# Performance work log

Hardware: AMD Instinct MI355X
Metric: run time of the kernel (lower is better)

## Reference

```python
import jax, jax.numpy as jnp
import numpy as np


def setup_inputs() -> dict:
    key = jax.random.key(0)
    k1, k2, k3 = jax.random.split(key, 3)
    B, C_in, H, W = 16, 256, 64, 64
    C_out, KH, KW = 256, 3, 3
    x = jax.random.normal(k1, (B, C_in, H, W), dtype=jnp.float32)
    # kaiming-uniform-like scale for realism
    fan_in = C_in * KH * KW
    bound = 1.0 / np.sqrt(fan_in)
    weights = jax.random.normal(k2, (C_out, C_in, KH, KW), dtype=jnp.float32) * bound
    bias = jax.random.uniform(k3, (C_out,), dtype=jnp.float32, minval=-bound, maxval=bound)
    return {"x": x, "weights": weights, "bias": bias}


def reference(x, weights, bias):
    # Conv2dApproximation with approximation_enable=False is an exact conv2d:
    # input is unfolded to [B, C*kh*kw, oh, ow], weights to [C_out, C*kh*kw],
    # and the MultiApp kernel performs the exact MAC (see exact matmul backward).
    # stride=(1,1), padding=(0,0), dilation=(1,1) per init_kwargs.
    out = jax.lax.conv_general_dilated(
        x, weights,
        window_strides=(1, 1),
        padding=((0, 0), (0, 0)),
        rhs_dilation=(1, 1),
        dimension_numbers=("NCHW", "OIHW", "NCHW"),
    )
    return out + bias[None, :, None, None]
```

## Files before the change

### kernel.cpp

```cpp
#include <hip/hip_runtime.h>
#include <stdint.h>

typedef short short8 __attribute__((ext_vector_type(8)));
typedef float f32x4 __attribute__((ext_vector_type(4)));

#define AS1 __attribute__((address_space(1)))
#define AS3 __attribute__((address_space(3)))

__device__ __forceinline__ void gl_lds16(const void* g, void* l) {
  __builtin_amdgcn_global_load_lds((const AS1 unsigned int*)g,
                                   (AS3 unsigned int*)l, 16, 0, 0);
}

__device__ __forceinline__ unsigned short f2bf(float f) {
  union { float f; unsigned int u; } v; v.f = f;
  return (unsigned short)((v.u + (((v.u >> 16) & 1u) + 0x7fffu)) >> 16);
}

__global__ __launch_bounds__(256) void xpose_kernel(const float* __restrict__ x,
                                                    unsigned short* __restrict__ xt) {
  __shared__ float tile[64][68];
  const int bid = blockIdx.x;
  const int cchunk = bid & 3;
  const int y = (bid >> 2) & 63;
  const int b = bid >> 8;
  const int t = threadIdx.x;
  const int ci0 = cchunk * 64;

  const int cc = t >> 2;
  const int xo = (t & 3) * 16;
  const float* src = x + (((size_t)(b * 256 + ci0 + cc) * 64 + y) * 64 + xo);
  float4 v0 = ((const float4*)src)[0];
  float4 v1 = ((const float4*)src)[1];
  float4 v2 = ((const float4*)src)[2];
  float4 v3 = ((const float4*)src)[3];
  *(float4*)&tile[cc][xo + 0]  = v0;
  *(float4*)&tile[cc][xo + 4]  = v1;
  *(float4*)&tile[cc][xo + 8]  = v2;
  *(float4*)&tile[cc][xo + 12] = v3;
  __syncthreads();

  const int xpos = t >> 2;
  const int ccg = (t & 3) * 16;
  unsigned int pk[8];
#pragma unroll
  for (int e = 0; e < 8; ++e) {
    unsigned int lo = f2bf(tile[ccg + 2 * e][xpos]);
    unsigned int hi = f2bf(tile[ccg + 2 * e + 1][xpos]);
    pk[e] = lo | (hi << 16);
  }
  unsigned short* dst = xt + ((size_t)(b * 4096 + y * 64 + xpos) * 256 + ci0 + ccg);
  uint4 w0; w0.x = pk[0]; w0.y = pk[1]; w0.z = pk[2]; w0.w = pk[3];
  uint4 w1; w1.x = pk[4]; w1.y = pk[5]; w1.z = pk[6]; w1.w = pk[7];
  ((uint4*)dst)[0] = w0;
  ((uint4*)dst)[1] = w1;
}

__global__ __launch_bounds__(256) void wpack_kernel(const float* __restrict__ w,
                                                    unsigned short* __restrict__ wrp) {
  const int idx = blockIdx.x * 256 + threadIdx.x;
  const int ci = idx & 255;
  const int co = (idx >> 8) & 255;
  const int p = idx >> 16;
  wrp[idx] = f2bf(w[(size_t)(co * 256 + ci) * 9 + p]);
}

__global__ __launch_bounds__(512, 2) void conv_8ph(
    const unsigned short* __restrict__ xt,
    const unsigned short* __restrict__ wrp,
    const float* __restrict__ bias,
    float* __restrict__ out) {
  __shared__ unsigned short lds[2][32768];

  const int tid = threadIdx.x;
  const int lane = tid & 63;
  const int wv = tid >> 6;
  const int wm = wv >> 2;
  const int wn = wv & 3;
  const int bid = blockIdx.x;
  const int tile = (bid & 7) * 32 + (bid >> 3);
  const int b = tile >> 4;
  const int oh0 = (tile & 15) * 4;

  const int crow = tid >> 3;
  const int cslot = tid & 7;
  const int sw = cslot ^ (crow & 7);
  const unsigned short* gAbase = wrp + (size_t)crow * 256 + sw * 8;
  const unsigned short* gBbase[4];
#pragma unroll
  for (int cb = 0; cb < 4; ++cb) {
    const int y = min(oh0 + cb, 61);
    const int x = min(crow, 61);
    gBbase[cb] = xt + ((size_t)(b * 64 + y) * 64 + x) * 256 + sw * 8;
  }
  const unsigned dst_rc = crow * 64 + cslot * 8;

  const int l15 = lane & 15;
  int s8[2];
  s8[0] = (((lane >> 4)) ^ (lane & 7)) * 8;
  s8[1] = (((lane >> 4) + 4) ^ (lane & 7)) * 8;
  int arow[8], brow[4];
#pragma unroll
  for (int a = 0; a < 8; ++a)
    arow[a] = (wm * 128 + (a >> 2) * 64 + (a & 3) * 16 + l15) * 64;
#pragma unroll
  for (int n = 0; n < 4; ++n)
    brow[n] = 16384 + (wn * 64 + n * 16 + l15) * 64;

  auto stageA = [&](int kt2, int c, unsigned short* bufp) {
    const int tap = kt2 >> 2, ci0 = (kt2 & 3) * 64;
    gl_lds16(gAbase + tap * 65536 + c * 16384 + ci0, bufp + c * 4096 + dst_rc);
  };
  auto stageB = [&](int kt2, int cb, unsigned short* bufp) {
    const int tap = kt2 >> 2, ci0 = (kt2 & 3) * 64;
    const int kh = (tap * 11) >> 5, kw = tap - kh * 3;
    gl_lds16(gBbase[cb] + (kh * 64 + kw) * 256 + ci0, bufp + (4 + cb) * 4096 + dst_rc);
  };

  f32x4 acc[8][4] = {};
  unsigned short* buf0 = &lds[0][0];
  unsigned short* buf1 = &lds[1][0];

  stageA(0, 0, buf0); stageA(0, 2, buf0); stageA(0, 1, buf0); stageA(0, 3, buf0);
  stageB(0, 2, buf0); stageB(0, 3, buf0); stageB(0, 0, buf0); stageB(0, 1, buf0);
  stageB(1, 0, buf1); stageB(1, 1, buf1);
  asm volatile("s_waitcnt vmcnt(2)" ::: "memory");
  __builtin_amdgcn_s_barrier();

  for (int kt = 0; kt < 36; ++kt) {
    unsigned short* buf = (kt & 1) ? buf1 : buf0;
    unsigned short* nbuf = (kt & 1) ? buf0 : buf1;
    short8 a0[4], a1[4], bb[4];

#pragma unroll
    for (int q = 0; q < 4; ++q) a0[q] = *(const short8*)(buf + arow[q] + s8[0]);
#pragma unroll
    for (int n = 0; n < 4; ++n) bb[n] = *(const short8*)(buf + brow[n] + s8[0]);
    if (kt < 35) { stageA(kt + 1, 0, nbuf); stageA(kt + 1, 2, nbuf); }
    __builtin_amdgcn_s_barrier();
    __builtin_amdgcn_s_setprio(1);
#pragma unroll
    for (int q = 0; q < 4; ++q)
#pragma unroll
      for (int n = 0; n < 4; ++n)
        acc[q][n] = __builtin_amdgcn_mfma_f32_16x16x32_bf16(a0[q], bb[n], acc[q][n], 0, 0, 0);
    __builtin_amdgcn_s_setprio(0);
    asm volatile("s_waitcnt lgkmcnt(0)" ::: "memory");
    __builtin_amdgcn_s_barrier();

#pragma unroll
    for (int q = 0; q < 4; ++q) a1[q] = *(const short8*)(buf + arow[4 + q] + s8[0]);
    if (kt < 35) { stageA(kt + 1, 1, nbuf); stageA(kt + 1, 3, nbuf); }
    __builtin_amdgcn_s_barrier();
    __builtin_amdgcn_s_setprio(1);
#pragma unroll
    for (int q = 0; q < 4; ++q)
#pragma unroll
      for (int n = 0; n < 4; ++n)
        acc[4 + q][n] = __builtin_amdgcn_mfma_f32_16x16x32_bf16(a1[q], bb[n], acc[4 + q][n], 0, 0, 0);
    __builtin_amdgcn_s_setprio(0);
    asm volatile("s_waitcnt lgkmcnt(0)" ::: "memory");
    __builtin_amdgcn_s_barrier();

#pragma unroll
    for (int q = 0; q < 4; ++q) a0[q] = *(const short8*)(buf + arow[q] + s8[1]);
#pragma unroll
    for (int n = 0; n < 4; ++n) bb[n] = *(const short8*)(buf + brow[n] + s8[1]);
    if (kt < 35) { stageB(kt + 1, 2, nbuf); stageB(kt + 1, 3, nbuf); }
    __builtin_amdgcn_s_barrier();
    __builtin_amdgcn_s_setprio(1);
#pragma unroll
    for (int q = 0; q < 4; ++q)
#pragma unroll
      for (int n = 0; n < 4; ++n)
        acc[q][n] = __builtin_amdgcn_mfma_f32_16x16x32_bf16(a0[q], bb[n], acc[q][n], 0, 0, 0);
    __builtin_amdgcn_s_setprio(0);
    asm volatile("s_waitcnt lgkmcnt(0)" ::: "memory");
    __builtin_amdgcn_s_barrier();

#pragma unroll
    for (int q = 0; q < 4; ++q) a1[q] = *(const short8*)(buf + arow[4 + q] + s8[1]);
    if (kt < 34) { stageB(kt + 2, 0, buf); stageB(kt + 2, 1, buf); }
    __builtin_amdgcn_s_barrier();
    __builtin_amdgcn_s_setprio(1);
#pragma unroll
    for (int q = 0; q < 4; ++q)
#pragma unroll
      for (int n = 0; n < 4; ++n)
        acc[4 + q][n] = __builtin_amdgcn_mfma_f32_16x16x32_bf16(a1[q], bb[n], acc[4 + q][n], 0, 0, 0);
    __builtin_amdgcn_s_setprio(0);
    asm volatile("s_waitcnt lgkmcnt(0)" ::: "memory");
    if (kt < 34)       asm volatile("s_waitcnt vmcnt(2)" ::: "memory");
    else if (kt == 34) asm volatile("s_waitcnt vmcnt(0)" ::: "memory");
    __builtin_amdgcn_s_barrier();
  }

  const int rb = (lane >> 4) * 4;
  const int colp = lane & 15;
#pragma unroll
  for (int a = 0; a < 8; ++a) {
    const int co = wm * 128 + (a >> 2) * 64 + (a & 3) * 16 + rb;
    float bv[4];
#pragma unroll
    for (int j = 0; j < 4; ++j) bv[j] = bias[co + j];
#pragma unroll
    for (int n = 0; n < 4; ++n) {
      const int px = wn * 64 + n * 16 + colp;
      const int prow = px >> 6, ow = px & 63;
      const int oh = oh0 + prow;
      if (ow < 62 && oh < 62) {
#pragma unroll
        for (int j = 0; j < 4; ++j)
          out[((size_t)(b * 256 + co + j) * 62 + oh) * 62 + ow] = acc[a][n][j] + bv[j];
      }
    }
  }
}

__global__ __launch_bounds__(256) void conv_naive(const float* __restrict__ x,
                                                  const float* __restrict__ wgt,
                                                  const float* __restrict__ bias,
                                                  float* __restrict__ out) {
  const size_t idx = (size_t)blockIdx.x * 256 + threadIdx.x;
  if (idx >= (size_t)16 * 256 * 62 * 62) return;
  const int ow = (int)(idx % 62);
  size_t r = idx / 62;
  const int oh = (int)(r % 62); r /= 62;
  const int co = (int)(r % 256);
  const int b = (int)(r / 256);
  float s = bias[co];
  for (int ci = 0; ci < 256; ++ci) {
    const float* xp = x + ((size_t)(b * 256 + ci) * 64 + oh) * 64 + ow;
    const float* wp = wgt + (size_t)(co * 256 + ci) * 9;
#pragma unroll
    for (int kh = 0; kh < 3; ++kh)
#pragma unroll
      for (int kw = 0; kw < 3; ++kw)
        s += xp[kh * 64 + kw] * wp[kh * 3 + kw];
  }
  out[idx] = s;
}

extern "C" void kernel_launch(void* const* d_in, const int* in_sizes, int n_in,
                              void* d_out, int out_size, void* d_ws, size_t ws_size,
                              hipStream_t stream) {
  const float* x = (const float*)d_in[0];
  const float* wgt = (const float*)d_in[1];
  const float* bias = (const float*)d_in[2];
  float* out = (float*)d_out;

  const size_t xt_elems = (size_t)16 * 64 * 64 * 256;
  const size_t wr_elems = (size_t)9 * 256 * 256;
  const size_t need = (xt_elems + wr_elems) * sizeof(unsigned short);

  if (ws_size < need) {
    conv_naive<<<61504, 256, 0, stream>>>(x, wgt, bias, out);
    return;
  }

  unsigned short* xt = (unsigned short*)d_ws;
  unsigned short* wrp = xt + xt_elems;

  xpose_kernel<<<4096, 256, 0, stream>>>(x, xt);
  wpack_kernel<<<2304, 256, 0, stream>>>(wgt, wrp);
  conv_8ph<<<256, 512, 0, stream>>>(xt, wrp, bias, out);
}
```

Measured before the change: 97.53 us.

## Load conv B operand directly into registers and triple-buffer A in LDS

The input-activation (B) fragments now go straight from global memory into registers, each wave fetching its own pixels, and are double-buffered two k-tiles ahead. Only the weight (A) tile is still staged in LDS, now across three rotating buffers. This cuts LDS traffic and drops the sync points from four barriers per k-tile to one, letting MFMA issue run with fewer stalls. In exchange, waves that share the same B columns fetch them redundantly from cache, two register buffers of B fragments add pressure under the 2-block launch bound, and the vmcnt accounting has to match the new load counts exactly.

```diff
diff --git a/kernel.cpp b/kernel.cpp
--- a/kernel.cpp
+++ b/kernel.cpp
@@ -65,12 +65,12 @@
   wrp[idx] = f2bf(w[(size_t)(co * 256 + ci) * 9 + p]);
 }
 
-__global__ __launch_bounds__(512, 2) void conv_8ph(
+__global__ __launch_bounds__(512, 2) void conv_breg(
     const unsigned short* __restrict__ xt,
     const unsigned short* __restrict__ wrp,
     const float* __restrict__ bias,
     float* __restrict__ out) {
-  __shared__ unsigned short lds[2][32768];
+  __shared__ unsigned short lds[3 * 16384];
 
   const int tid = threadIdx.x;
   const int lane = tid & 63;
@@ -86,113 +86,99 @@
   const int cslot = tid & 7;
   const int sw = cslot ^ (crow & 7);
   const unsigned short* gAbase = wrp + (size_t)crow * 256 + sw * 8;
-  const unsigned short* gBbase[4];
-#pragma unroll
-  for (int cb = 0; cb < 4; ++cb) {
-    const int y = min(oh0 + cb, 61);
-    const int x = min(crow, 61);
-    gBbase[cb] = xt + ((size_t)(b * 64 + y) * 64 + x) * 256 + sw * 8;
-  }
-  const unsigned dst_rc = crow * 64 + cslot * 8;
+  const unsigned dstA = crow * 64 + cslot * 8;
 
   const int l15 = lane & 15;
-  int s8[2];
-  s8[0] = (((lane >> 4)) ^ (lane & 7)) * 8;
-  s8[1] = (((lane >> 4) + 4) ^ (lane & 7)) * 8;
-  int arow[8], brow[4];
-#pragma unroll
-  for (int a = 0; a < 8; ++a)
-    arow[a] = (wm * 128 + (a >> 2) * 64 + (a & 3) * 16 + l15) * 64;
-#pragma unroll
-  for (int n = 0; n < 4; ++n)
-    brow[n] = 16384 + (wn * 64 + n * 16 + l15) * 64;
-
-  auto stageA = [&](int kt2, int c, unsigned short* bufp) {
+  const int kq = lane >> 4;
+  const int s8k0 = ((kq) ^ (lane & 7)) * 8;
+  const int s8k1 = ((kq + 4) ^ (lane & 7)) * 8;
+
+  const unsigned short* pB[4];
+#pragma unroll
+  for (int n = 0; n < 4; ++n) {
+    const int px = wn * 64 + n * 16 + l15;
+    const int y = min(oh0 + (px >> 6), 61);
+    const int xc = min(px & 63, 61);
+    pB[n] = xt + ((size_t)(b * 64 + y) * 64 + xc) * 256 + kq * 8;
+  }
+
+  auto stageA = [&](int kt2, unsigned short* pst) {
     const int tap = kt2 >> 2, ci0 = (kt2 & 3) * 64;
-    gl_lds16(gAbase + tap * 65536 + c * 16384 + ci0, bufp + c * 4096 + dst_rc);
+    const unsigned short* g = gAbase + tap * 65536 + ci0;
+#pragma unroll
+    for (int c = 0; c < 4; ++c)
+      gl_lds16(g + c * 16384, pst + c * 4096 + dstA);
   };
-  auto stageB = [&](int kt2, int cb, unsigned short* bufp) {
+  auto loadB = [&](int kt2, short8 (&dst)[4][2]) {
     const int tap = kt2 >> 2, ci0 = (kt2 & 3) * 64;
     const int kh = (tap * 11) >> 5, kw = tap - kh * 3;
-    gl_lds16(gBbase[cb] + (kh * 64 + kw) * 256 + ci0, bufp + (4 + cb) * 4096 + dst_rc);
+    const int boff = (kh * 64 + kw) * 256 + ci0;
+#pragma unroll
+    for (int n = 0; n < 4; ++n) {
+      dst[n][0] = *(const short8*)(pB[n] + boff);
+      dst[n][1] = *(const short8*)(pB[n] + boff + 32);
+    }
   };
 
   f32x4 acc[8][4] = {};
-  unsigned short* buf0 = &lds[0][0];
-  unsigned short* buf1 = &lds[1][0];
-
-  stageA(0, 0, buf0); stageA(0, 2, buf0); stageA(0, 1, buf0); stageA(0, 3, buf0);
-  stageB(0, 2, buf0); stageB(0, 3, buf0); stageB(0, 0, buf0); stageB(0, 1, buf0);
-  stageB(1, 0, buf1); stageB(1, 1, buf1);
-  asm volatile("s_waitcnt vmcnt(2)" ::: "memory");
-  __builtin_amdgcn_s_barrier();
-
-  for (int kt = 0; kt < 36; ++kt) {
-    unsigned short* buf = (kt & 1) ? buf1 : buf0;
-    unsigned short* nbuf = (kt & 1) ? buf0 : buf1;
-    short8 a0[4], a1[4], bb[4];
-
-#pragma unroll
-    for (int q = 0; q < 4; ++q) a0[q] = *(const short8*)(buf + arow[q] + s8[0]);
-#pragma unroll
-    for (int n = 0; n < 4; ++n) bb[n] = *(const short8*)(buf + brow[n] + s8[0]);
-    if (kt < 35) { stageA(kt + 1, 0, nbuf); stageA(kt + 1, 2, nbuf); }
-    __builtin_amdgcn_s_barrier();
-    __builtin_amdgcn_s_setprio(1);
-#pragma unroll
-    for (int q = 0; q < 4; ++q)
-#pragma unroll
-      for (int n = 0; n < 4; ++n)
-        acc[q][n] = __builtin_amdgcn_mfma_f32_16x16x32_bf16(a0[q], bb[n], acc[q][n], 0, 0, 0);
-    __builtin_amdgcn_s_setprio(0);
-    asm volatile("s_waitcnt lgkmcnt(0)" ::: "memory");
-    __builtin_amdgcn_s_barrier();
-
-#pragma unroll
-    for (int q = 0; q < 4; ++q) a1[q] = *(const short8*)(buf + arow[4 + q] + s8[0]);
-    if (kt < 35) { stageA(kt + 1, 1, nbuf); stageA(kt + 1, 3, nbuf); }
-    __builtin_amdgcn_s_barrier();
-    __builtin_amdgcn_s_setprio(1);
-#pragma unroll
-    for (int q = 0; q < 4; ++q)
-#pragma unroll
-      for (int n = 0; n < 4; ++n)
-        acc[4 + q][n] = __builtin_amdgcn_mfma_f32_16x16x32_bf16(a1[q], bb[n], acc[4 + q][n], 0, 0, 0);
-    __builtin_amdgcn_s_setprio(0);
-    asm volatile("s_waitcnt lgkmcnt(0)" ::: "memory");
-    __builtin_amdgcn_s_barrier();
-
-#pragma unroll
-    for (int q = 0; q < 4; ++q) a0[q] = *(const short8*)(buf + arow[q] + s8[1]);
-#pragma unroll
-    for (int n = 0; n < 4; ++n) bb[n] = *(const short8*)(buf + brow[n] + s8[1]);
-    if (kt < 35) { stageB(kt + 1, 2, nbuf); stageB(kt + 1, 3, nbuf); }
-    __builtin_amdgcn_s_barrier();
-    __builtin_amdgcn_s_setprio(1);
-#pragma unroll
-    for (int q = 0; q < 4; ++q)
-#pragma unroll
-      for (int n = 0; n < 4; ++n)
-        acc[q][n] = __builtin_amdgcn_mfma_f32_16x16x32_bf16(a0[q], bb[n], acc[q][n], 0, 0, 0);
-    __builtin_amdgcn_s_setprio(0);
-    asm volatile("s_waitcnt lgkmcnt(0)" ::: "memory");
-    __builtin_amdgcn_s_barrier();
-
-#pragma unroll
-    for (int q = 0; q < 4; ++q) a1[q] = *(const short8*)(buf + arow[4 + q] + s8[1]);
-    if (kt < 34) { stageB(kt + 2, 0, buf); stageB(kt + 2, 1, buf); }
-    __builtin_amdgcn_s_barrier();
-    __builtin_amdgcn_s_setprio(1);
-#pragma unroll
-    for (int q = 0; q < 4; ++q)
-#pragma unroll
-      for (int n = 0; n < 4; ++n)
-        acc[4 + q][n] = __builtin_amdgcn_mfma_f32_16x16x32_bf16(a1[q], bb[n], acc[4 + q][n], 0, 0, 0);
-    __builtin_amdgcn_s_setprio(0);
-    asm volatile("s_waitcnt lgkmcnt(0)" ::: "memory");
-    if (kt < 34)       asm volatile("s_waitcnt vmcnt(2)" ::: "memory");
+
+  auto ktile = [&](int kt, short8 (&bc)[4][2], unsigned short* pcur,
+                   unsigned short* pst) {
+    short8 af[4];
+#pragma unroll
+    for (int q = 0; q < 4; ++q)
+      af[q] = *(const short8*)(pcur + (wm * 128 + q * 16 + l15) * 64 + s8k0);
+#pragma unroll
+    for (int q = 0; q < 4; ++q)
+#pragma unroll
+      for (int n = 0; n < 4; ++n)
+        acc[q][n] = __builtin_amdgcn_mfma_f32_16x16x32_bf16(af[q], bc[n][0], acc[q][n], 0, 0, 0);
+#pragma unroll
+    for (int q = 0; q < 4; ++q)
+      af[q] = *(const short8*)(pcur + (wm * 128 + 64 + q * 16 + l15) * 64 + s8k0);
+#pragma unroll
+    for (int q = 0; q < 4; ++q)
+#pragma unroll
+      for (int n = 0; n < 4; ++n)
+        acc[4 + q][n] = __builtin_amdgcn_mfma_f32_16x16x32_bf16(af[q], bc[n][0], acc[4 + q][n], 0, 0, 0);
+#pragma unroll
+    for (int q = 0; q < 4; ++q)
+      af[q] = *(const short8*)(pcur + (wm * 128 + q * 16 + l15) * 64 + s8k1);
+#pragma unroll
+    for (int q = 0; q < 4; ++q)
+#pragma unroll
+      for (int n = 0; n < 4; ++n)
+        acc[q][n] = __builtin_amdgcn_mfma_f32_16x16x32_bf16(af[q], bc[n][1], acc[q][n], 0, 0, 0);
+#pragma unroll
+    for (int q = 0; q < 4; ++q)
+      af[q] = *(const short8*)(pcur + (wm * 128 + 64 + q * 16 + l15) * 64 + s8k1);
+#pragma unroll
+    for (int q = 0; q < 4; ++q)
+#pragma unroll
+      for (int n = 0; n < 4; ++n)
+        acc[4 + q][n] = __builtin_amdgcn_mfma_f32_16x16x32_bf16(af[q], bc[n][1], acc[4 + q][n], 0, 0, 0);
+    if (kt < 34) { stageA(kt + 2, pst); loadB(kt + 2, bc); }
+    if (kt < 34)       asm volatile("s_waitcnt vmcnt(12)" ::: "memory");
     else if (kt == 34) asm volatile("s_waitcnt vmcnt(0)" ::: "memory");
     __builtin_amdgcn_s_barrier();
+  };
+
+  short8 bb0[4][2], bb1[4][2];
+  unsigned short* p0 = lds;
+  unsigned short* p1 = lds + 16384;
+  unsigned short* p2 = lds + 32768;
+
+  stageA(0, p0); loadB(0, bb0);
+  asm volatile("" ::: "memory");
+  stageA(1, p1); loadB(1, bb1);
+  asm volatile("s_waitcnt vmcnt(12)" ::: "memory");
+  __builtin_amdgcn_s_barrier();
+
+  for (int t = 0; t < 18; ++t) {
+    ktile(2 * t, bb0, p0, p2);
+    unsigned short* tmp = p0; p0 = p1; p1 = p2; p2 = tmp;
+    ktile(2 * t + 1, bb1, p0, p2);
+    tmp = p0; p0 = p1; p1 = p2; p2 = tmp;
   }
 
   const int rb = (lane >> 4) * 4;
@@ -263,5 +249,5 @@
 
   xpose_kernel<<<4096, 256, 0, stream>>>(x, xt);
   wpack_kernel<<<2304, 256, 0, stream>>>(wgt, wrp);
-  conv_8ph<<<256, 512, 0, stream>>>(xt, wrp, bias, out);
-}
+  conv_breg<<<256, 512, 0, stream>>>(xt, wrp, bias, out);
+}
```

Result: slower. 109.2 us (+12.0%).
